# Performance work log

Hardware: AMD Instinct MI355X
Metric: run time of the kernel (lower is better)

## Reference

```python
import jax, jax.numpy as jnp
import numpy as np

BRANCH = 8
DEPTH = 4
BATCH = 8192


def _build_tree(b=BRANCH, depth=DEPTH):
    level_sizes = [b ** l for l in range(depth + 1)]
    offsets = np.cumsum([0] + level_sizes)
    E = int(offsets[-1])  # 4681 total nodes (edges)
    parent = np.full(E, -1, dtype=np.int64)
    for l in range(1, depth + 1):
        idx = np.arange(level_sizes[l])
        parent[offsets[l] + idx] = offsets[l - 1] + idx // b
    # Each node's softmax group = its parent's children group; root -> group 0 ('ROOT').
    # Internal nodes occupy indices [0, offsets[depth]), so group id = parent+1.
    seg = np.where(parent < 0, 0, parent + 1).astype(np.int32)
    # path_onehot[i, j] = 1 iff j is an ancestor of i or i itself (path to root)
    P = np.zeros((E, E), dtype=np.float32)
    rows = np.arange(E)
    cur = rows.copy()
    for _ in range(depth + 1):
        P[rows, cur] = 1.0
        cur = np.where(parent[cur] < 0, cur, parent[cur])
    P[rows, cur] = 1.0  # root
    return seg, P


def setup_inputs() -> dict:
    key = jax.random.key(0)
    seg, P = _build_tree()
    E = seg.shape[0]
    inputs = jax.random.normal(key, (BATCH, E), dtype=jnp.float32)
    return {
        "inputs": inputs,
        "segment_ids": jnp.asarray(seg),
        "path_onehot": jnp.asarray(P),
    }


def _cascade_log_softmax(inputs, segment_ids, num_segments):
    # inputs: [B, E]; segmented (per-group) log_softmax along the edge axis.
    xT = inputs.T  # [E, B]
    mx = jax.ops.segment_max(xT, segment_ids, num_segments=num_segments)  # [S, B]
    shifted = xT - mx[segment_ids]
    lse = jnp.log(jax.ops.segment_sum(jnp.exp(shifted), segment_ids,
                                      num_segments=num_segments))  # [S, B]
    return (shifted - lse[segment_ids]).T  # [B, E]


def reference(inputs, segment_ids, path_onehot):
    # final_probabilities: product of conditionals along root-to-node paths
    num_segments = int(jnp.max(segment_ids)) + 1
    log_prob = _cascade_log_softmax(inputs, segment_ids, num_segments)  # [B, E]
    # log p(node) = sum of conditional log-probs over ancestors-or-self
    return jnp.exp(log_prob @ path_onehot.T)  # [B, E]
```

## Files before the change

kernel.cpp:

```cpp
#include <hip/hip_runtime.h>


constexpr int E  = 4681;
constexpr int NG = 585;

__global__ __launch_bounds__(256) void cascade_kernel(const float* __restrict__ in,
                                                      float* __restrict__ out) {
    __shared__ float xs[E];
    __shared__ float dj[NG];
    const int tid  = threadIdx.x;
    const int lane = tid & 63;
    const long long rowbase = (long long)blockIdx.x * (long long)E;
    const float* __restrict__ rin  = in  + rowbase;
    float* __restrict__       rout = out + rowbase;

    const int s   = (int)((4 - (rowbase & 3)) & 3);
    const int nv4 = (E - s) >> 2;
    const float* vbase = rin + s;
    const int wbase = tid - lane;
    #pragma unroll
    for (int u = 0; u < 5; ++u) {
        const int f = u * 256 + wbase;
        if (f < nv4) {
            const int idx = f + lane;
            if (idx < nv4) {
                __builtin_amdgcn_global_load_lds(
                    (const __attribute__((address_space(1))) void*)(vbase + 4 * idx),
                    (__attribute__((address_space(3))) void*)(&xs[s + 4 * f]),
                    16, 0, 0);
            }
        }
    }
    if (tid < s) xs[tid] = rin[tid];
    const int t0 = s + 4 * nv4;
    if (tid < E - t0) xs[t0 + tid] = rin[t0 + tid];
    __syncthreads();

    for (int j = tid; j < E - 1; j += 256) {
        const float v = xs[j + 1];
        float m = v;
        m = fmaxf(m, __shfl_xor(m, 1));
        m = fmaxf(m, __shfl_xor(m, 2));
        m = fmaxf(m, __shfl_xor(m, 4));
        float e = __expf(v - m);
        e += __shfl_xor(e, 1);
        e += __shfl_xor(e, 2);
        e += __shfl_xor(e, 4);
        if ((j & 7) == 0) dj[j >> 3] = -m - __logf(e);
    }
    __syncthreads();

    if (tid >= 1 && tid <= 8) dj[tid] += xs[tid] + dj[0];
    __syncthreads();
    if (tid >= 9 && tid < 73) dj[tid] += xs[tid] + dj[(tid - 1) >> 3];
    __syncthreads();
    for (int p = 73 + tid; p < NG; p += 256) dj[p] += xs[p] + dj[(p - 1) >> 3];
    __syncthreads();

    for (int j = tid; j < E - 1; j += 256) {
        rout[j + 1] = __expf(xs[j + 1] + dj[j >> 3]);
    }
    if (tid == 0) rout[0] = 1.0f;
}

extern "C" void kernel_launch(void* const* d_in, const int* in_sizes, int n_in,
                              void* d_out, int out_size, void* d_ws, size_t ws_size,
                              hipStream_t stream) {
    const float* in = (const float*)d_in[0];
    float* out = (float*)d_out;
    const int B = in_sizes[0] / E;
    cascade_kernel<<<B, 256, 0, stream>>>(in, out);
}
```

Before: 305.7 us.

## Keep row groups in registers and replace level-wise LDS scan with ancestor walks

Each thread now loads whole 8-element sibling groups straight into registers with vector loads specialised per row alignment, instead of staging the full row through LDS. Group log-sum-exp is computed in registers without shuffles. The four barrier-separated level passes become independent walks up at most three ancestors, so only two barriers remain. Outputs are written from registers with aligned vector stores. This trades less LDS traffic and synchronisation for higher register pressure, more template code and partly uncoalesced per-thread strided loads.

```diff
diff --git a/kernel.cpp b/kernel.cpp
--- a/kernel.cpp
+++ b/kernel.cpp
@@ -4,63 +4,157 @@
 constexpr int E  = 4681;
 constexpr int NG = 585;
 
-__global__ __launch_bounds__(256) void cascade_kernel(const float* __restrict__ in,
-                                                      float* __restrict__ out) {
-    __shared__ float xs[E];
-    __shared__ float dj[NG];
-    const int tid  = threadIdx.x;
-    const int lane = tid & 63;
-    const long long rowbase = (long long)blockIdx.x * (long long)E;
-    const float* __restrict__ rin  = in  + rowbase;
-    float* __restrict__       rout = out + rowbase;
+__device__ __forceinline__ int xslot(int p) { return p + (p >> 3); }
+constexpr int XN = 658;
 
-    const int s   = (int)((4 - (rowbase & 3)) & 3);
-    const int nv4 = (E - s) >> 2;
-    const float* vbase = rin + s;
-    const int wbase = tid - lane;
+template<int R>
+__device__ __forceinline__ void loadw(const float* __restrict__ rin, int g, float w[9]) {
+    if (g == 584) {
+        #pragma unroll
+        for (int k = 0; k < 9; ++k) w[k] = rin[4672 + k];
+        return;
+    }
+    if (R == 0) {
+        const float4 A = *(const float4*)(rin + 8 * g);
+        const float4 B = *(const float4*)(rin + 8 * g + 4);
+        w[0] = A.x; w[1] = A.y; w[2] = A.z; w[3] = A.w;
+        w[4] = B.x; w[5] = B.y; w[6] = B.z; w[7] = B.w;
+        w[8] = rin[8 * g + 8];
+    } else {
+        const float4 A = *(const float4*)(rin + 8 * g - R);
+        const float4 B = *(const float4*)(rin + 8 * g - R + 4);
+        const float4 C = *(const float4*)(rin + 8 * g - R + 8);
+        const float L[12] = {A.x, A.y, A.z, A.w, B.x, B.y, B.z, B.w, C.x, C.y, C.z, C.w};
+        #pragma unroll
+        for (int k = 0; k < 9; ++k) w[k] = L[R + k];
+    }
+}
+
+template<int R>
+__device__ __forceinline__ void storew(float* __restrict__ rout, int g, const float y[9]) {
+    if (g == 584) {
+        #pragma unroll
+        for (int k = 0; k < 9; ++k) rout[4672 + k] = y[k];
+        return;
+    }
+    float* q = rout + 8 * g;
+    if (R == 0) {
+        *(float4*)(q)     = make_float4(y[0], y[1], y[2], y[3]);
+        *(float4*)(q + 4) = make_float4(y[4], y[5], y[6], y[7]);
+    } else if (R == 1) {
+        q[0] = y[0];
+        *(float2*)(q + 1) = make_float2(y[1], y[2]);
+        *(float4*)(q + 3) = make_float4(y[3], y[4], y[5], y[6]);
+        q[7] = y[7];
+    } else if (R == 2) {
+        *(float2*)(q)     = make_float2(y[0], y[1]);
+        *(float4*)(q + 2) = make_float4(y[2], y[3], y[4], y[5]);
+        *(float2*)(q + 6) = make_float2(y[6], y[7]);
+    } else {
+        q[0] = y[0];
+        *(float4*)(q + 1) = make_float4(y[1], y[2], y[3], y[4]);
+        *(float2*)(q + 5) = make_float2(y[5], y[6]);
+        q[7] = y[7];
+    }
+}
+
+__device__ __forceinline__ float group_adj(const float w[9]) {
+    float m = w[1];
     #pragma unroll
-    for (int u = 0; u < 5; ++u) {
-        const int f = u * 256 + wbase;
-        if (f < nv4) {
-            const int idx = f + lane;
-            if (idx < nv4) {
-                __builtin_amdgcn_global_load_lds(
-                    (const __attribute__((address_space(1))) void*)(vbase + 4 * idx),
-                    (__attribute__((address_space(3))) void*)(&xs[s + 4 * f]),
-                    16, 0, 0);
-            }
+    for (int k = 2; k < 9; ++k) m = fmaxf(m, w[k]);
+    float s = 0.0f;
+    #pragma unroll
+    for (int k = 1; k < 9; ++k) s += __expf(w[k] - m);
+    return -m - __logf(s);
+}
+
+__device__ __forceinline__ float walkD(int g, const float* adj, const float* xn) {
+    float D = adj[g];
+    int q = g;
+    #pragma unroll
+    for (int it = 0; it < 3; ++it) {
+        if (q > 0) {
+            D += xn[xslot(q)];
+            q = (q - 1) >> 3;
+            D += adj[q];
         }
     }
-    if (tid < s) xs[tid] = rin[tid];
-    const int t0 = s + 4 * nv4;
-    if (tid < E - t0) xs[t0 + tid] = rin[t0 + tid];
-    __syncthreads();
+    return D;
+}
 
-    for (int j = tid; j < E - 1; j += 256) {
-        const float v = xs[j + 1];
-        float m = v;
-        m = fmaxf(m, __shfl_xor(m, 1));
-        m = fmaxf(m, __shfl_xor(m, 2));
-        m = fmaxf(m, __shfl_xor(m, 4));
-        float e = __expf(v - m);
-        e += __shfl_xor(e, 1);
-        e += __shfl_xor(e, 2);
-        e += __shfl_xor(e, 4);
-        if ((j & 7) == 0) dj[j >> 3] = -m - __logf(e);
+template<int R>
+__device__ __forceinline__ void row_body(const float* __restrict__ rin,
+                                         float* __restrict__ rout,
+                                         float* adj, float* dj, float* xn, int tid) {
+    const int g0 = tid, g1 = tid + 256, g2 = tid + 512;
+    const bool h2 = (g2 < NG);
+    float w0[9], w1[9], w2[9];
+    loadw<R>(rin, g0, w0);
+    loadw<R>(rin, g1, w1);
+    if (h2) loadw<R>(rin, g2, w2);
+
+    adj[g0] = group_adj(w0);
+    adj[g1] = group_adj(w1);
+    if (h2) adj[g2] = group_adj(w2);
+
+    if (g0 <= 73) {
+        #pragma unroll
+        for (int k = 0; k < 8; ++k) {
+            const int node = 8 * g0 + k;
+            if (node >= 1 && node <= 584) xn[xslot(node)] = w0[k];
+        }
     }
     __syncthreads();
 
-    if (tid >= 1 && tid <= 8) dj[tid] += xs[tid] + dj[0];
-    __syncthreads();
-    if (tid >= 9 && tid < 73) dj[tid] += xs[tid] + dj[(tid - 1) >> 3];
-    __syncthreads();
-    for (int p = 73 + tid; p < NG; p += 256) dj[p] += xs[p] + dj[(p - 1) >> 3];
+    const float D0 = walkD(g0, adj, xn);
+    const float D1 = walkD(g1, adj, xn);
+    const float D2 = h2 ? walkD(g2, adj, xn) : 0.0f;
+    dj[g0] = D0; dj[g1] = D1;
+    if (h2) dj[g2] = D2;
     __syncthreads();
 
-    for (int j = tid; j < E - 1; j += 256) {
-        rout[j + 1] = __expf(xs[j + 1] + dj[j >> 3]);
+    float y[9];
+    {
+        const float Dp = (g0 > 0) ? dj[g0 - 1] : 0.0f;
+        y[0] = (g0 == 0) ? 1.0f : __expf(w0[0] + Dp);
+        #pragma unroll
+        for (int k = 1; k < 8; ++k) y[k] = __expf(w0[k] + D0);
+        y[8] = 0.0f;
+        storew<R>(rout, g0, y);
     }
-    if (tid == 0) rout[0] = 1.0f;
+    {
+        const float Dp = dj[g1 - 1];
+        y[0] = __expf(w1[0] + Dp);
+        #pragma unroll
+        for (int k = 1; k < 8; ++k) y[k] = __expf(w1[k] + D1);
+        y[8] = 0.0f;
+        storew<R>(rout, g1, y);
+    }
+    if (h2) {
+        const float Dp = dj[g2 - 1];
+        y[0] = __expf(w2[0] + Dp);
+        #pragma unroll
+        for (int k = 1; k < 8; ++k) y[k] = __expf(w2[k] + D2);
+        y[8] = __expf(w2[8] + D2);
+        storew<R>(rout, g2, y);
+    }
+}
+
+__global__ __launch_bounds__(256, 4) void cascade_kernel(const float* __restrict__ in,
+                                                         float* __restrict__ out) {
+    __shared__ float adj[NG];
+    __shared__ float dj[NG];
+    __shared__ float xn[XN];
+    const int tid = threadIdx.x;
+    const long long rowbase = (long long)blockIdx.x * (long long)E;
+    const float* rin = in + rowbase;
+    float* rout = out + rowbase;
+    switch ((int)(rowbase & 3)) {
+        case 0: row_body<0>(rin, rout, adj, dj, xn, tid); break;
+        case 1: row_body<1>(rin, rout, adj, dj, xn, tid); break;
+        case 2: row_body<2>(rin, rout, adj, dj, xn, tid); break;
+        case 3: row_body<3>(rin, rout, adj, dj, xn, tid); break;
+    }
 }
 
 extern "C" void kernel_launch(void* const* d_in, const int* in_sizes, int n_in,
```

Result: faster. 298.6 us (-2.3%).
